# Kernel tuning notes

Measured on AMD Instinct MI355X. Metric: run time of the kernel, lower is better.

The kernel has to match this reference:

```python
import jax, jax.numpy as jnp
import numpy as np

D_MODEL = 256
NUM_HEADS = 8
DEPTH = D_MODEL // NUM_HEADS
NEG_BIG = -1e9


def setup_inputs() -> dict:
    key = jax.random.key(0)
    ks = jax.random.split(key, 8)
    B, S = 4, 2048
    inp = {
        "v": jax.random.normal(ks[0], (B, S, D_MODEL), dtype=jnp.float32),
        "k": jax.random.normal(ks[1], (B, S, D_MODEL), dtype=jnp.float32),
        "q": jax.random.normal(ks[2], (B, S, D_MODEL), dtype=jnp.float32),
        "mask": jnp.ones((B, S), dtype=jnp.float32),
        # kernel_size-1 Conv1D without bias == dense projection (d_in, d_out)
        "Wq": jax.random.normal(ks[3], (D_MODEL, D_MODEL), dtype=jnp.float32) * 0.05,
        "Wk": jax.random.normal(ks[4], (D_MODEL, D_MODEL), dtype=jnp.float32) * 0.05,
        "Wv": jax.random.normal(ks[5], (D_MODEL, D_MODEL), dtype=jnp.float32) * 0.05,
        "Wo": jax.random.normal(ks[6], (D_MODEL, D_MODEL), dtype=jnp.float32) * 0.05,
    }
    return inp


def _split_heads(x):
    # (B, S, d_model) -> (B, H, S, depth)
    B, S, _ = x.shape
    return x.reshape(B, S, NUM_HEADS, DEPTH).transpose(0, 2, 1, 3)


def reference(v, k, q, mask, Wq, Wk, Wv, Wo):
    B, S, _ = q.shape
    qh = _split_heads(q @ Wq)  # (B,H,Sq,depth)
    kh = _split_heads(k @ Wk)  # (B,H,Sk,depth)
    vh = _split_heads(v @ Wv)  # (B,H,Sk,depth)

    scale = 1.0 / jnp.sqrt(jnp.asarray(DEPTH, dtype=jnp.float32))
    logits = jnp.einsum("bhqd,bhkd->bhqk", qh, kh) * scale  # (B,H,Sq,Sk)
    mask_att = mask[:, None, None, :]  # broadcast over heads and query dim
    logits = logits + (1.0 - mask_att) * NEG_BIG
    attn = jax.nn.softmax(logits, axis=-1)  # (B,H,Sq,Sk)

    ctx = jnp.einsum("bhqk,bhkd->bhqd", attn, vh)  # (B,H,Sq,depth)
    concat = ctx.transpose(0, 2, 1, 3).reshape(B, S, D_MODEL)
    out = concat @ Wo
    return (out, attn)
```

## Files before the change

### kernel.cpp

```cpp
#include <hip/hip_runtime.h>

#define BB 4
#define HH 8
#define SS 2048
#define DD 32
#define DMODEL 256
#define NEG_BIG_F (-1000000000.0f)
#define SCALE 0.17677669529663687f

typedef short short8 __attribute__((ext_vector_type(8)));
typedef float float4_ __attribute__((ext_vector_type(4)));

__device__ __forceinline__ unsigned short f2bf(float x) {
  unsigned u = __float_as_uint(x);
  u += 0x7FFFu + ((u >> 16) & 1u);
  return (unsigned short)(u >> 16);
}

__global__ __launch_bounds__(256) void proj_kernel(
    const float* __restrict__ q, const float* __restrict__ k,
    const float* __restrict__ v,
    const float* __restrict__ Wq, const float* __restrict__ Wk,
    const float* __restrict__ Wv,
    unsigned short* __restrict__ qh, unsigned short* __restrict__ kh,
    unsigned short* __restrict__ vh) {
  int z = blockIdx.z;
  const float* src = (z == 0) ? q : (z == 1) ? k : v;
  const float* W = (z == 0) ? Wq : (z == 1) ? Wk : Wv;
  unsigned short* dst = (z == 0) ? qh : (z == 1) ? kh : vh;

  int w = threadIdx.x >> 6;
  int lane = threadIdx.x & 63;
  int l16 = lane & 15;
  int g = lane >> 4;

  int row = blockIdx.x * 64 + w * 16 + l16;
  int n0 = blockIdx.y * 64;

  float4_ z4 = {0.f, 0.f, 0.f, 0.f};
  float4_ acc[4] = {z4, z4, z4, z4};

  for (int k0 = 0; k0 < DMODEL; k0 += 32) {
    const float* ap = src + (size_t)row * DMODEL + k0 + 8 * g;
    short8 a;
#pragma unroll
    for (int j = 0; j < 8; ++j) a[j] = (short)f2bf(ap[j]);
#pragma unroll
    for (int cb = 0; cb < 4; ++cb) {
      int n = n0 + cb * 16 + l16;
      short8 bfr;
#pragma unroll
      for (int j = 0; j < 8; ++j)
        bfr[j] = (short)f2bf(W[(size_t)(k0 + 8 * g + j) * DMODEL + n]);
      acc[cb] = __builtin_amdgcn_mfma_f32_16x16x32_bf16(a, bfr, acc[cb], 0, 0, 0);
    }
  }

  int rowbase = blockIdx.x * 64 + w * 16 + 4 * g;
#pragma unroll
  for (int cb = 0; cb < 4; ++cb) {
#pragma unroll
    for (int rr = 0; rr < 4; ++rr) {
      int r = rowbase + rr;
      int c = n0 + cb * 16 + l16;
      int b = r >> 11, s = r & (SS - 1);
      int h = c >> 5, d = c & 31;
      dst[(((size_t)(b * HH + h) * SS + s) * DD) + d] = f2bf(acc[cb][rr]);
    }
  }
}

__global__ __launch_bounds__(256) void stats_kernel(
    const unsigned short* __restrict__ qh, const unsigned short* __restrict__ kh,
    const float* __restrict__ mask, float* __restrict__ m_arr,
    float* __restrict__ l_arr) {
  __shared__ float bias[SS];
  int bh = blockIdx.y;
  int b = bh >> 3;
  for (int i = threadIdx.x; i < SS; i += 256)
    bias[i] = (1.0f - mask[(size_t)b * SS + i]) * NEG_BIG_F;
  __syncthreads();

  int w = threadIdx.x >> 6, lane = threadIdx.x & 63, l16 = lane & 15,
      g = lane >> 4;
  int q0 = blockIdx.x * 64 + w * 16;

  short8 qa = *(const short8*)(qh + ((size_t)bh * SS + q0 + l16) * DD + 8 * g);

  float m[4], l[4];
#pragma unroll
  for (int i = 0; i < 4; ++i) {
    m[i] = -INFINITY;
    l[i] = 0.f;
  }

  const unsigned short* kbase = kh + (size_t)bh * SS * DD;
  float4_ z4 = {0.f, 0.f, 0.f, 0.f};
  for (int k0 = 0; k0 < SS; k0 += 16) {
    short8 kf = *(const short8*)(kbase + (size_t)(k0 + l16) * DD + 8 * g);
    float4_ r = __builtin_amdgcn_mfma_f32_16x16x32_bf16(qa, kf, z4, 0, 0, 0);
    float bk = bias[k0 + l16];
#pragma unroll
    for (int rr = 0; rr < 4; ++rr) {
      float t = fmaf(r[rr], SCALE, bk);
      float nm = fmaxf(m[rr], t);
      l[rr] = l[rr] * __expf(m[rr] - nm) + __expf(t - nm);
      m[rr] = nm;
    }
  }
#pragma unroll
  for (int off = 1; off < 16; off <<= 1) {
#pragma unroll
    for (int rr = 0; rr < 4; ++rr) {
      float om = __shfl_xor(m[rr], off);
      float ol = __shfl_xor(l[rr], off);
      float nm = fmaxf(m[rr], om);
      l[rr] = l[rr] * __expf(m[rr] - nm) + ol * __expf(om - nm);
      m[rr] = nm;
    }
  }
  if (l16 == 0) {
#pragma unroll
    for (int rr = 0; rr < 4; ++rr) {
      size_t idx = (size_t)bh * SS + q0 + 4 * g + rr;
      m_arr[idx] = m[rr];
      l_arr[idx] = l[rr];
    }
  }
}

__global__ __launch_bounds__(256) void emit_kernel(
    const unsigned short* __restrict__ qh, const unsigned short* __restrict__ kh,
    const unsigned short* __restrict__ vh, const float* __restrict__ mask,
    const float* __restrict__ m_arr, const float* __restrict__ l_arr,
    float* __restrict__ attn_out, unsigned short* __restrict__ concat) {
  __shared__ float bias[SS];
  __shared__ unsigned short vt[32][72];
  __shared__ unsigned short at[4][16][72];

  int bh = blockIdx.y;
  int b = bh >> 3, h = bh & 7;
  for (int i = threadIdx.x; i < SS; i += 256)
    bias[i] = (1.0f - mask[(size_t)b * SS + i]) * NEG_BIG_F;

  int w = threadIdx.x >> 6, lane = threadIdx.x & 63, l16 = lane & 15,
      g = lane >> 4;
  int q0 = blockIdx.x * 64 + w * 16;

  short8 qa = *(const short8*)(qh + ((size_t)bh * SS + q0 + l16) * DD + 8 * g);

  float mr[4], rl[4];
#pragma unroll
  for (int rr = 0; rr < 4; ++rr) {
    size_t idx = (size_t)bh * SS + q0 + 4 * g + rr;
    mr[rr] = m_arr[idx];
    rl[rr] = 1.0f / l_arr[idx];
  }

  const unsigned short* kbase = kh + (size_t)bh * SS * DD;
  const unsigned short* vbase = vh + (size_t)bh * SS * DD;
  float* arow = attn_out + (size_t)bh * SS * SS;

  float4_ z4 = {0.f, 0.f, 0.f, 0.f};
  float4_ acc0 = z4, acc1 = z4;

  int vr = threadIdx.x >> 2;
  int dseg = (threadIdx.x & 3) * 8;

  for (int kb = 0; kb < SS; kb += 64) {
    __syncthreads();
    {
      short8 vv = *(const short8*)(vbase + (size_t)(kb + vr) * DD + dseg);
#pragma unroll
      for (int j = 0; j < 8; ++j) vt[dseg + j][vr] = (unsigned short)vv[j];
    }
    __syncthreads();

#pragma unroll
    for (int ks = 0; ks < 2; ++ks) {
#pragma unroll
      for (int kt = 0; kt < 2; ++kt) {
        int k0 = kb + ks * 32 + kt * 16;
        short8 kf = *(const short8*)(kbase + (size_t)(k0 + l16) * DD + 8 * g);
        float4_ r = __builtin_amdgcn_mfma_f32_16x16x32_bf16(qa, kf, z4, 0, 0, 0);
        float bk = bias[k0 + l16];
#pragma unroll
        for (int rr = 0; rr < 4; ++rr) {
          float t = fmaf(r[rr], SCALE, bk);
          float p = __expf(t - mr[rr]) * rl[rr];
          arow[(size_t)(q0 + 4 * g + rr) * SS + k0 + l16] = p;
          at[w][4 * g + rr][ks * 32 + kt * 16 + l16] = f2bf(p);
        }
      }
      short8 pa = *(const short8*)&at[w][l16][ks * 32 + 8 * g];
      short8 b0 = *(const short8*)&vt[l16][ks * 32 + 8 * g];
      short8 b1 = *(const short8*)&vt[16 + l16][ks * 32 + 8 * g];
      acc0 = __builtin_amdgcn_mfma_f32_16x16x32_bf16(pa, b0, acc0, 0, 0, 0);
      acc1 = __builtin_amdgcn_mfma_f32_16x16x32_bf16(pa, b1, acc1, 0, 0, 0);
    }
  }

#pragma unroll
  for (int rr = 0; rr < 4; ++rr) {
    int s = q0 + 4 * g + rr;
    size_t base = ((size_t)b * SS + s) * DMODEL + h * DD;
    concat[base + l16] = f2bf(acc0[rr]);
    concat[base + 16 + l16] = f2bf(acc1[rr]);
  }
}

__global__ __launch_bounds__(256) void outgemm_kernel(
    const unsigned short* __restrict__ concat, const float* __restrict__ Wo,
    float* __restrict__ out) {
  int w = threadIdx.x >> 6, lane = threadIdx.x & 63, l16 = lane & 15,
      g = lane >> 4;
  int row = blockIdx.x * 64 + w * 16 + l16;
  int n0 = blockIdx.y * 64;
  float4_ z4 = {0.f, 0.f, 0.f, 0.f};
  float4_ acc[4] = {z4, z4, z4, z4};
  for (int k0 = 0; k0 < DMODEL; k0 += 32) {
    short8 a = *(const short8*)(concat + (size_t)row * DMODEL + k0 + 8 * g);
#pragma unroll
    for (int cb = 0; cb < 4; ++cb) {
      int n = n0 + cb * 16 + l16;
      short8 bfr;
#pragma unroll
      for (int j = 0; j < 8; ++j)
        bfr[j] = (short)f2bf(Wo[(size_t)(k0 + 8 * g + j) * DMODEL + n]);
      acc[cb] = __builtin_amdgcn_mfma_f32_16x16x32_bf16(a, bfr, acc[cb], 0, 0, 0);
    }
  }
  int rowbase = blockIdx.x * 64 + w * 16 + 4 * g;
#pragma unroll
  for (int cb = 0; cb < 4; ++cb)
#pragma unroll
    for (int rr = 0; rr < 4; ++rr)
      out[(size_t)(rowbase + rr) * DMODEL + n0 + cb * 16 + l16] = acc[cb][rr];
}

extern "C" void kernel_launch(void* const* d_in, const int* in_sizes, int n_in,
                              void* d_out, int out_size, void* d_ws,
                              size_t ws_size, hipStream_t stream) {
  const float* v = (const float*)d_in[0];
  const float* k = (const float*)d_in[1];
  const float* q = (const float*)d_in[2];
  const float* mask = (const float*)d_in[3];
  const float* Wq = (const float*)d_in[4];
  const float* Wk = (const float*)d_in[5];
  const float* Wv = (const float*)d_in[6];
  const float* Wo = (const float*)d_in[7];

  float* out = (float*)d_out;
  float* attn = out + (size_t)BB * SS * DMODEL;

  const size_t NH = (size_t)BB * HH * SS * DD;
  unsigned short* qh = (unsigned short*)d_ws;
  unsigned short* kh = qh + NH;
  unsigned short* vh = kh + NH;
  unsigned short* concat = vh + NH;
  float* m_arr = (float*)(concat + (size_t)BB * SS * DMODEL);
  float* l_arr = m_arr + (size_t)BB * HH * SS;

  proj_kernel<<<dim3(128, 4, 3), 256, 0, stream>>>(q, k, v, Wq, Wk, Wv, qh, kh,
                                                   vh);
  stats_kernel<<<dim3(32, 32), 256, 0, stream>>>(qh, kh, mask, m_arr, l_arr);
  emit_kernel<<<dim3(32, 32), 256, 0, stream>>>(qh, kh, vh, mask, m_arr, l_arr,
                                                attn, concat);
  outgemm_kernel<<<dim3(128, 4), 256, 0, stream>>>(concat, Wo, out);
}
```

Before: 259.1 us.

## Fuse stats and emit kernels, pre-transpose weights to bf16, nontemporal attn stores

Merges the softmax-statistics and probability-emit kernels into one kernel that keeps row max and sum in registers, removing a launch and the m/l round trip through global memory. Adds a prep kernel that transposes and converts all four weight matrices to bf16 once, so the projection GEMMs load contiguous short8 weight fragments instead of doing strided scalar loads and converting them. Also vectorises the activation loads, replaces the online-softmax update with a branch that needs one exp per element, unrolls the stats loop by two, and writes the large attention matrix with nontemporal stores. The branchy update may diverge within a wavefront, and the extra prep kernel adds a launch.

```diff
diff --git a/kernel.cpp b/kernel.cpp
--- a/kernel.cpp
+++ b/kernel.cpp
@@ -17,23 +17,35 @@
   return (unsigned short)(u >> 16);
 }
 
+__global__ __launch_bounds__(256) void prep_w(
+    const float* __restrict__ Wq, const float* __restrict__ Wk,
+    const float* __restrict__ Wv, const float* __restrict__ Wo,
+    unsigned short* __restrict__ wt) {
+  __shared__ float tile[32][33];
+  int z = blockIdx.z;
+  const float* W = (z == 0) ? Wq : (z == 1) ? Wk : (z == 2) ? Wv : Wo;
+  unsigned short* dst = wt + (size_t)z * DMODEL * DMODEL;
+  int k0 = blockIdx.x * 32, n0 = blockIdx.y * 32;
+  int tx = threadIdx.x & 31, ty = threadIdx.x >> 5;
+  for (int r = ty; r < 32; r += 8)
+    tile[r][tx] = W[(size_t)(k0 + r) * DMODEL + n0 + tx];
+  __syncthreads();
+  for (int r = ty; r < 32; r += 8)
+    dst[(size_t)(n0 + r) * DMODEL + k0 + tx] = f2bf(tile[tx][r]);
+}
+
 __global__ __launch_bounds__(256) void proj_kernel(
     const float* __restrict__ q, const float* __restrict__ k,
-    const float* __restrict__ v,
-    const float* __restrict__ Wq, const float* __restrict__ Wk,
-    const float* __restrict__ Wv,
+    const float* __restrict__ v, const unsigned short* __restrict__ wt,
     unsigned short* __restrict__ qh, unsigned short* __restrict__ kh,
     unsigned short* __restrict__ vh) {
   int z = blockIdx.z;
   const float* src = (z == 0) ? q : (z == 1) ? k : v;
-  const float* W = (z == 0) ? Wq : (z == 1) ? Wk : Wv;
+  const unsigned short* Wt = wt + (size_t)z * DMODEL * DMODEL;
   unsigned short* dst = (z == 0) ? qh : (z == 1) ? kh : vh;
 
-  int w = threadIdx.x >> 6;
-  int lane = threadIdx.x & 63;
-  int l16 = lane & 15;
-  int g = lane >> 4;
-
+  int w = threadIdx.x >> 6, lane = threadIdx.x & 63, l16 = lane & 15,
+      g = lane >> 4;
   int row = blockIdx.x * 64 + w * 16 + l16;
   int n0 = blockIdx.y * 64;
 
@@ -41,17 +53,18 @@
   float4_ acc[4] = {z4, z4, z4, z4};
 
   for (int k0 = 0; k0 < DMODEL; k0 += 32) {
-    const float* ap = src + (size_t)row * DMODEL + k0 + 8 * g;
+    const float4_* ap = (const float4_*)(src + (size_t)row * DMODEL + k0 + 8 * g);
+    float4_ a0 = ap[0], a1 = ap[1];
     short8 a;
 #pragma unroll
-    for (int j = 0; j < 8; ++j) a[j] = (short)f2bf(ap[j]);
+    for (int j = 0; j < 4; ++j) {
+      a[j] = (short)f2bf(a0[j]);
+      a[4 + j] = (short)f2bf(a1[j]);
+    }
 #pragma unroll
     for (int cb = 0; cb < 4; ++cb) {
       int n = n0 + cb * 16 + l16;
-      short8 bfr;
-#pragma unroll
-      for (int j = 0; j < 8; ++j)
-        bfr[j] = (short)f2bf(W[(size_t)(k0 + 8 * g + j) * DMODEL + n]);
+      short8 bfr = *(const short8*)(Wt + (size_t)n * DMODEL + k0 + 8 * g);
       acc[cb] = __builtin_amdgcn_mfma_f32_16x16x32_bf16(a, bfr, acc[cb], 0, 0, 0);
     }
   }
@@ -70,13 +83,16 @@
   }
 }
 
-__global__ __launch_bounds__(256) void stats_kernel(
+__global__ __launch_bounds__(256) void fused_attn(
     const unsigned short* __restrict__ qh, const unsigned short* __restrict__ kh,
-    const float* __restrict__ mask, float* __restrict__ m_arr,
-    float* __restrict__ l_arr) {
+    const unsigned short* __restrict__ vh, const float* __restrict__ mask,
+    float* __restrict__ attn_out, unsigned short* __restrict__ concat) {
   __shared__ float bias[SS];
+  __shared__ unsigned short vt[32][72];
+  __shared__ unsigned short at[4][16][72];
+
   int bh = blockIdx.y;
-  int b = bh >> 3;
+  int b = bh >> 3, h = bh & 7;
   for (int i = threadIdx.x; i < SS; i += 256)
     bias[i] = (1.0f - mask[(size_t)b * SS + i]) * NEG_BIG_F;
   __syncthreads();
@@ -87,15 +103,17 @@
 
   short8 qa = *(const short8*)(qh + ((size_t)bh * SS + q0 + l16) * DD + 8 * g);
 
+  const unsigned short* kbase = kh + (size_t)bh * SS * DD;
+  const unsigned short* vbase = vh + (size_t)bh * SS * DD;
+  float4_ z4 = {0.f, 0.f, 0.f, 0.f};
+
   float m[4], l[4];
 #pragma unroll
   for (int i = 0; i < 4; ++i) {
     m[i] = -INFINITY;
     l[i] = 0.f;
   }
-
-  const unsigned short* kbase = kh + (size_t)bh * SS * DD;
-  float4_ z4 = {0.f, 0.f, 0.f, 0.f};
+#pragma unroll 2
   for (int k0 = 0; k0 < SS; k0 += 16) {
     short8 kf = *(const short8*)(kbase + (size_t)(k0 + l16) * DD + 8 * g);
     float4_ r = __builtin_amdgcn_mfma_f32_16x16x32_bf16(qa, kf, z4, 0, 0, 0);
@@ -103,9 +121,12 @@
 #pragma unroll
     for (int rr = 0; rr < 4; ++rr) {
       float t = fmaf(r[rr], SCALE, bk);
-      float nm = fmaxf(m[rr], t);
-      l[rr] = l[rr] * __expf(m[rr] - nm) + __expf(t - nm);
-      m[rr] = nm;
+      if (t > m[rr]) {
+        l[rr] = l[rr] * __expf(m[rr] - t) + 1.0f;
+        m[rr] = t;
+      } else {
+        l[rr] += __expf(t - m[rr]);
+      }
     }
   }
 #pragma unroll
@@ -114,54 +135,19 @@
     for (int rr = 0; rr < 4; ++rr) {
       float om = __shfl_xor(m[rr], off);
       float ol = __shfl_xor(l[rr], off);
-      float nm = fmaxf(m[rr], om);
-      l[rr] = l[rr] * __expf(m[rr] - nm) + ol * __expf(om - nm);
-      m[rr] = nm;
-    }
-  }
-  if (l16 == 0) {
-#pragma unroll
-    for (int rr = 0; rr < 4; ++rr) {
-      size_t idx = (size_t)bh * SS + q0 + 4 * g + rr;
-      m_arr[idx] = m[rr];
-      l_arr[idx] = l[rr];
-    }
-  }
-}
-
-__global__ __launch_bounds__(256) void emit_kernel(
-    const unsigned short* __restrict__ qh, const unsigned short* __restrict__ kh,
-    const unsigned short* __restrict__ vh, const float* __restrict__ mask,
-    const float* __restrict__ m_arr, const float* __restrict__ l_arr,
-    float* __restrict__ attn_out, unsigned short* __restrict__ concat) {
-  __shared__ float bias[SS];
-  __shared__ unsigned short vt[32][72];
-  __shared__ unsigned short at[4][16][72];
-
-  int bh = blockIdx.y;
-  int b = bh >> 3, h = bh & 7;
-  for (int i = threadIdx.x; i < SS; i += 256)
-    bias[i] = (1.0f - mask[(size_t)b * SS + i]) * NEG_BIG_F;
-
-  int w = threadIdx.x >> 6, lane = threadIdx.x & 63, l16 = lane & 15,
-      g = lane >> 4;
-  int q0 = blockIdx.x * 64 + w * 16;
-
-  short8 qa = *(const short8*)(qh + ((size_t)bh * SS + q0 + l16) * DD + 8 * g);
-
-  float mr[4], rl[4];
-#pragma unroll
-  for (int rr = 0; rr < 4; ++rr) {
-    size_t idx = (size_t)bh * SS + q0 + 4 * g + rr;
-    mr[rr] = m_arr[idx];
-    rl[rr] = 1.0f / l_arr[idx];
-  }
-
-  const unsigned short* kbase = kh + (size_t)bh * SS * DD;
-  const unsigned short* vbase = vh + (size_t)bh * SS * DD;
+      if (om > m[rr]) {
+        l[rr] = l[rr] * __expf(m[rr] - om) + ol;
+        m[rr] = om;
+      } else {
+        l[rr] += ol * __expf(om - m[rr]);
+      }
+    }
+  }
+  float rl[4];
+#pragma unroll
+  for (int rr = 0; rr < 4; ++rr) rl[rr] = 1.0f / l[rr];
+
   float* arow = attn_out + (size_t)bh * SS * SS;
-
-  float4_ z4 = {0.f, 0.f, 0.f, 0.f};
   float4_ acc0 = z4, acc1 = z4;
 
   int vr = threadIdx.x >> 2;
@@ -187,8 +173,9 @@
 #pragma unroll
         for (int rr = 0; rr < 4; ++rr) {
           float t = fmaf(r[rr], SCALE, bk);
-          float p = __expf(t - mr[rr]) * rl[rr];
-          arow[(size_t)(q0 + 4 * g + rr) * SS + k0 + l16] = p;
+          float p = __expf(t - m[rr]) * rl[rr];
+          __builtin_nontemporal_store(
+              p, &arow[(size_t)(q0 + 4 * g + rr) * SS + k0 + l16]);
           at[w][4 * g + rr][ks * 32 + kt * 16 + l16] = f2bf(p);
         }
       }
@@ -210,7 +197,8 @@
 }
 
 __global__ __launch_bounds__(256) void outgemm_kernel(
-    const unsigned short* __restrict__ concat, const float* __restrict__ Wo,
+    const unsigned short* __restrict__ concat,
+    const unsigned short* __restrict__ wot,
     float* __restrict__ out) {
   int w = threadIdx.x >> 6, lane = threadIdx.x & 63, l16 = lane & 15,
       g = lane >> 4;
@@ -223,10 +211,7 @@
 #pragma unroll
     for (int cb = 0; cb < 4; ++cb) {
       int n = n0 + cb * 16 + l16;
-      short8 bfr;
-#pragma unroll
-      for (int j = 0; j < 8; ++j)
-        bfr[j] = (short)f2bf(Wo[(size_t)(k0 + 8 * g + j) * DMODEL + n]);
+      short8 bfr = *(const short8*)(wot + (size_t)n * DMODEL + k0 + 8 * g);
       acc[cb] = __builtin_amdgcn_mfma_f32_16x16x32_bf16(a, bfr, acc[cb], 0, 0, 0);
     }
   }
@@ -258,13 +243,11 @@
   unsigned short* kh = qh + NH;
   unsigned short* vh = kh + NH;
   unsigned short* concat = vh + NH;
-  float* m_arr = (float*)(concat + (size_t)BB * SS * DMODEL);
-  float* l_arr = m_arr + (size_t)BB * HH * SS;
-
-  proj_kernel<<<dim3(128, 4, 3), 256, 0, stream>>>(q, k, v, Wq, Wk, Wv, qh, kh,
-                                                   vh);
-  stats_kernel<<<dim3(32, 32), 256, 0, stream>>>(qh, kh, mask, m_arr, l_arr);
-  emit_kernel<<<dim3(32, 32), 256, 0, stream>>>(qh, kh, vh, mask, m_arr, l_arr,
-                                                attn, concat);
-  outgemm_kernel<<<dim3(128, 4), 256, 0, stream>>>(concat, Wo, out);
-}
+  unsigned short* wt = concat + (size_t)BB * SS * DMODEL;
+
+  prep_w<<<dim3(8, 8, 4), 256, 0, stream>>>(Wq, Wk, Wv, Wo, wt);
+  proj_kernel<<<dim3(128, 4, 3), 256, 0, stream>>>(q, k, v, wt, qh, kh, vh);
+  fused_attn<<<dim3(32, 32), 256, 0, stream>>>(qh, kh, vh, mask, attn, concat);
+  outgemm_kernel<<<dim3(128, 4), 256, 0, stream>>>(
+      concat, wt + (size_t)3 * DMODEL * DMODEL, out);
+}
```

Result: slower. 277.8 us (+7.2%).
